# Performance work log

Measured on AMD Instinct MI355X. Metric: run time of the kernel, lower is better.

The kernel has to match this reference:

```python
import jax, jax.numpy as jnp
import numpy as np

N, BIT, NUM_CLASSES = 512, 64, 100
ALPHA = 5.0   # config['alpha']
LAM = 1.0     # config['lambda']


def setup_inputs() -> dict:
    key = jax.random.key(0)
    k_u, k_lbl = jax.random.split(key)
    u = jax.random.normal(k_u, (N, BIT), dtype=jnp.float32)
    labels = jax.random.randint(k_lbl, (N,), 0, NUM_CLASSES)
    y = jax.nn.one_hot(labels, NUM_CLASSES, dtype=jnp.float32)  # [N, C]
    return {"u": u, "y": y}


def reference(u, y):
    dt = u.dtype
    ip = u @ u.T                       # [N, N] inner products
    s = (y @ y.T) > 0                  # [N, N] similarity mask (bool)
    pos = s.astype(dt)                 # positive-pair mask per row
    neg = 1.0 - pos                    # negative-pair mask per row
    npos = pos.sum(axis=1)             # [N]
    nneg = neg.sum(axis=1)             # [N]
    valid = (npos > 0) & (nneg > 0)    # rows contributing to loss1

    # triple[r, p, n] = ip[r, p] - ip[r, n] - alpha, clamped as in the original
    triple = jnp.clip(ip[:, :, None] - ip[:, None, :] - ALPHA, -100.0, 50.0)  # [N, N, N]
    # per-element loss: -(t - log(1 + exp(t)))  (clamp keeps exp finite)
    f = jnp.log1p(jnp.exp(triple)) - triple

    w = pos[:, :, None] * neg[:, None, :]            # valid (pos, neg) pair mask
    pair_count = jnp.maximum(npos * nneg, 1.0)       # avoid div-by-zero on skipped rows
    row_loss = (f * w).sum(axis=(1, 2)) / pair_count  # masked mean per row

    count = valid.sum().astype(dt)
    loss1 = jnp.where(count > 0,
                      jnp.where(valid, row_loss, 0.0).sum() / jnp.maximum(count, 1.0),
                      jnp.asarray(0.0, dt))
    loss2 = LAM * jnp.mean((u - jnp.sign(u)) ** 2)   # quantization penalty
    return loss1 + loss2
```

## Files before the change

### kernel.cpp

```cpp
#include <hip/hip_runtime.h>
#include <hip/hip_bf16.h>
#include <math.h>

#define N 512
#define BIT 64
#define NUM_CLASSES 100
#define ALPHA 5.0f
#define LAM 1.0f


__global__ void label_kernel(const float* __restrict__ y,
                             int* __restrict__ labels) {
    int r = blockIdx.x * 64 + threadIdx.x;
    const float* yr = y + (size_t)r * NUM_CLASSES;
    int lbl = 0;
    for (int c = 0; c < NUM_CLASSES; ++c) {
        if (yr[c] > 0.5f) lbl = c;
    }
    labels[r] = lbl;
}

__global__ void fused_kernel(const float* __restrict__ u,
                             const int* __restrict__ labels,
                             float* __restrict__ acc,
                             int* __restrict__ ctr,
                             float* __restrict__ out) {
    int r = blockIdx.x;
    int tid = threadIdx.x;

    __shared__ float ur[BIT];
    __shared__ float d[N];
    __shared__ int   lab[N];
    __shared__ int   poslist[N];
    __shared__ int   npos_s;
    __shared__ float wsum[4];

    if (tid == 0) npos_s = 0;
    if (tid < BIT) ur[tid] = u[(size_t)r * BIT + tid];
    for (int i = tid; i < N; i += 256) lab[i] = labels[i];
    __syncthreads();

    float4 urv[16];
    const float4* urf = (const float4*)ur;
    #pragma unroll
    for (int k = 0; k < 16; ++k) urv[k] = urf[k];

    for (int n = tid; n < N; n += 256) {
        const float4* un = (const float4*)(u + (size_t)n * BIT);
        float s = 0.0f;
        #pragma unroll
        for (int k = 0; k < 16; ++k) {
            float4 a = un[k];
            float4 b = urv[k];
            s += a.x * b.x + a.y * b.y + a.z * b.z + a.w * b.w;
        }
        d[n] = s;
    }

    if (tid < 64) {
        float v = ur[tid];
        float sg = (v > 0.0f) ? 1.0f : ((v < 0.0f) ? -1.0f : 0.0f);
        float dd = v - sg;
        float s2 = dd * dd;
        for (int off = 32; off > 0; off >>= 1) s2 += __shfl_down(s2, off, 64);
        if (tid == 0) atomicAdd(&acc[2], s2);
    }
    __syncthreads();

    int lr = lab[r];
    for (int i = tid; i < N; i += 256) {
        if (lab[i] == lr) {
            int idx = atomicAdd(&npos_s, 1);
            poslist[idx] = i;
        }
    }
    __syncthreads();

    int npos = npos_s;
    int nneg = N - npos;

    float fsum = 0.0f;
    for (int pi = 0; pi < npos; ++pi) {
        float dp = d[poslist[pi]];
        for (int n = tid; n < N; n += 256) {
            if (lab[n] != lr) {
                float t = dp - d[n] - ALPHA;
                t = fminf(fmaxf(t, -100.0f), 50.0f);
                float f = (t > 0.0f) ? log1pf(expf(-t))
                                     : (log1pf(expf(t)) - t);
                fsum += f;
            }
        }
    }

    for (int off = 32; off > 0; off >>= 1) fsum += __shfl_down(fsum, off, 64);
    if ((tid & 63) == 0) wsum[tid >> 6] = fsum;
    __syncthreads();

    if (tid == 0) {
        float total = wsum[0] + wsum[1] + wsum[2] + wsum[3];
        bool valid = (npos > 0) && (nneg > 0);
        float pair_count = fmaxf((float)npos * (float)nneg, 1.0f);
        if (valid) {
            atomicAdd(&acc[0], total / pair_count);
            atomicAdd(&acc[1], 1.0f);
        }
        __threadfence();
        int done = atomicAdd(ctr, 1);
        if (done == N - 1) {
            float s1  = atomicAdd(&acc[0], 0.0f);
            float cnt = atomicAdd(&acc[1], 0.0f);
            float s2  = atomicAdd(&acc[2], 0.0f);
            float loss1 = (cnt > 0.0f) ? (s1 / fmaxf(cnt, 1.0f)) : 0.0f;
            out[0] = loss1 + LAM * s2 / (float)(N * BIT);
        }
    }
}

extern "C" void kernel_launch(void* const* d_in, const int* in_sizes, int n_in,
                              void* d_out, int out_size, void* d_ws, size_t ws_size,
                              hipStream_t stream) {
    const float* u = (const float*)d_in[0];
    const float* y = (const float*)d_in[1];
    float* out = (float*)d_out;

    char* ws = (char*)d_ws;
    float* acc    = (float*)ws;
    int*   ctr    = (int*)(ws + 12);
    int*   labels = (int*)(ws + 64);

    hipMemsetAsync(ws, 0, 64, stream);

    label_kernel<<<8, 64, 0, stream>>>(y, labels);
    fused_kernel<<<N, 256, 0, stream>>>(u, labels, acc, ctr, out);
}
```

Baseline: 93.05 us.

## Fuse label extraction into main kernel and replace atomics with finish kernel

Each block now computes all row labels itself from the one-hot y matrix, using a weighted sum of class indices, which removes the separate label kernel. Per-row losses, valid flags and quantization sums are written to workspace, and a single-block finish kernel reduces them. This removes the memset, the global atomics and the last-block counter. In exchange, every block re-reads the full 512x100 label matrix, and the label trick assumes strictly one-hot rows.

```diff
diff --git a/kernel.cpp b/kernel.cpp
--- a/kernel.cpp
+++ b/kernel.cpp
@@ -9,22 +9,11 @@
 #define LAM 1.0f
 
 
-__global__ void label_kernel(const float* __restrict__ y,
-                             int* __restrict__ labels) {
-    int r = blockIdx.x * 64 + threadIdx.x;
-    const float* yr = y + (size_t)r * NUM_CLASSES;
-    int lbl = 0;
-    for (int c = 0; c < NUM_CLASSES; ++c) {
-        if (yr[c] > 0.5f) lbl = c;
-    }
-    labels[r] = lbl;
-}
-
 __global__ void fused_kernel(const float* __restrict__ u,
-                             const int* __restrict__ labels,
-                             float* __restrict__ acc,
-                             int* __restrict__ ctr,
-                             float* __restrict__ out) {
+                             const float* __restrict__ y,
+                             float* __restrict__ row_loss,
+                             float* __restrict__ valid,
+                             float* __restrict__ sum2) {
     int r = blockIdx.x;
     int tid = threadIdx.x;
 
@@ -37,7 +26,20 @@
 
     if (tid == 0) npos_s = 0;
     if (tid < BIT) ur[tid] = u[(size_t)r * BIT + tid];
-    for (int i = tid; i < N; i += 256) lab[i] = labels[i];
+
+    #pragma unroll
+    for (int rep = 0; rep < 2; ++rep) {
+        int n = tid + rep * 256;
+        const float4* yn = (const float4*)(y + (size_t)n * NUM_CLASSES);
+        float s = 0.0f;
+        #pragma unroll
+        for (int j = 0; j < NUM_CLASSES / 4; ++j) {
+            float4 a = yn[j];
+            float c0 = (float)(4 * j);
+            s += a.x * c0 + a.y * (c0 + 1.0f) + a.z * (c0 + 2.0f) + a.w * (c0 + 3.0f);
+        }
+        lab[n] = (int)(s + 0.5f);
+    }
     __syncthreads();
 
     float4 urv[16];
@@ -63,7 +65,7 @@
         float dd = v - sg;
         float s2 = dd * dd;
         for (int off = 32; off > 0; off >>= 1) s2 += __shfl_down(s2, off, 64);
-        if (tid == 0) atomicAdd(&acc[2], s2);
+        if (tid == 0) sum2[r] = s2;
     }
     __syncthreads();
 
@@ -99,21 +101,39 @@
 
     if (tid == 0) {
         float total = wsum[0] + wsum[1] + wsum[2] + wsum[3];
-        bool valid = (npos > 0) && (nneg > 0);
+        bool v = (npos > 0) && (nneg > 0);
         float pair_count = fmaxf((float)npos * (float)nneg, 1.0f);
-        if (valid) {
-            atomicAdd(&acc[0], total / pair_count);
-            atomicAdd(&acc[1], 1.0f);
-        }
-        __threadfence();
-        int done = atomicAdd(ctr, 1);
-        if (done == N - 1) {
-            float s1  = atomicAdd(&acc[0], 0.0f);
-            float cnt = atomicAdd(&acc[1], 0.0f);
-            float s2  = atomicAdd(&acc[2], 0.0f);
-            float loss1 = (cnt > 0.0f) ? (s1 / fmaxf(cnt, 1.0f)) : 0.0f;
-            out[0] = loss1 + LAM * s2 / (float)(N * BIT);
-        }
+        row_loss[r] = v ? (total / pair_count) : 0.0f;
+        valid[r]   = v ? 1.0f : 0.0f;
+    }
+}
+
+__global__ void finish_kernel(const float* __restrict__ row_loss,
+                              const float* __restrict__ valid,
+                              const float* __restrict__ sum2,
+                              float* __restrict__ out) {
+    int tid = threadIdx.x;
+    __shared__ float w0[8], w1[8], w2[8];
+
+    float a = row_loss[tid];
+    float b = valid[tid];
+    float c = sum2[tid];
+    for (int off = 32; off > 0; off >>= 1) {
+        a += __shfl_down(a, off, 64);
+        b += __shfl_down(b, off, 64);
+        c += __shfl_down(c, off, 64);
+    }
+    if ((tid & 63) == 0) {
+        int w = tid >> 6;
+        w0[w] = a; w1[w] = b; w2[w] = c;
+    }
+    __syncthreads();
+    if (tid == 0) {
+        float s1 = 0.0f, cnt = 0.0f, s2 = 0.0f;
+        #pragma unroll
+        for (int w = 0; w < 8; ++w) { s1 += w0[w]; cnt += w1[w]; s2 += w2[w]; }
+        float loss1 = (cnt > 0.0f) ? (s1 / fmaxf(cnt, 1.0f)) : 0.0f;
+        out[0] = loss1 + LAM * s2 / (float)(N * BIT);
     }
 }
 
@@ -125,12 +145,10 @@
     float* out = (float*)d_out;
 
     char* ws = (char*)d_ws;
-    float* acc    = (float*)ws;
-    int*   ctr    = (int*)(ws + 12);
-    int*   labels = (int*)(ws + 64);
+    float* row_loss = (float*)ws;
+    float* valid    = (float*)(ws + N * sizeof(float));
+    float* sum2     = (float*)(ws + 2 * N * sizeof(float));
 
-    hipMemsetAsync(ws, 0, 64, stream);
-
-    label_kernel<<<8, 64, 0, stream>>>(y, labels);
-    fused_kernel<<<N, 256, 0, stream>>>(u, labels, acc, ctr, out);
+    fused_kernel<<<N, 256, 0, stream>>>(u, y, row_loss, valid, sum2);
+    finish_kernel<<<1, 512, 0, stream>>>(row_loss, valid, sum2, out);
 }
```

New measurement: 92.77 us. Within noise of the previous version (-0.3%).
